# Kernel tuning notes

Hardware: AMD Instinct MI355X
Metric: run time of the kernel (lower is better)

Reference implementation:

```python
import jax, jax.numpy as jnp
import numpy as np

B, N, C, H = 8, 1024, 1024, 16  # batch, seq, dim, heads
HID = 4 * C                     # mlp hidden (mlp_ratio=4.0)


def _ln(x, g, b, eps=1e-5):
    m = x.mean(-1, keepdims=True)
    v = ((x - m) ** 2).mean(-1, keepdims=True)
    return (x - m) / jnp.sqrt(v + eps) * g + b


def setup_inputs() -> dict:
    key = jax.random.key(0)
    ks = jax.random.split(key, 8)
    s = 0.02  # init scale
    f32 = jnp.float32
    return {
        "x": jax.random.normal(ks[0], (B, N, C), f32),
        "g1": jnp.ones((C,), f32), "b1": jnp.zeros((C,), f32),
        "Wq": jax.random.normal(ks[1], (C, C), f32) * s, "bq": jnp.zeros((C,), f32),
        "Wk": jax.random.normal(ks[2], (C, C), f32) * s, "bk": jnp.zeros((C,), f32),
        "Wv": jax.random.normal(ks[3], (C, C), f32) * s, "bv": jnp.zeros((C,), f32),
        "Wp": jax.random.normal(ks[4], (C, C), f32) * s, "bp": jnp.zeros((C,), f32),
        "g2": jnp.ones((C,), f32), "b2": jnp.zeros((C,), f32),
        "W1": jax.random.normal(ks[5], (C, HID), f32) * s, "c1": jnp.zeros((HID,), f32),
        "W2": jax.random.normal(ks[6], (HID, C), f32) * s, "c2": jnp.zeros((C,), f32),
    }


def reference(x, g1, b1, Wq, bq, Wk, bk, Wv, bv, Wp, bp, g2, b2, W1, c1, W2, c2):
    hd = C // H
    scale = hd ** -0.5
    # --- pre-norm self-attention ---
    h = _ln(x, g1, b1)
    # NOTE: faithful to source: direct reshape (B,N,C)->(B,H,N,hd), NOT the
    # standard reshape(B,N,H,hd).transpose -- the original code reshapes the
    # flat N*C block into H contiguous chunks of N*hd.
    q = (h @ Wq + bq).reshape(B, H, -1, hd)
    k = (h @ Wk + bk).reshape(B, H, -1, hd)
    v = (h @ Wv + bv).reshape(B, H, -1, hd)
    attn = jax.nn.softmax(jnp.einsum('bhnd,bhmd->bhnm', q, k) * scale, axis=-1)
    o = jnp.einsum('bhnm,bhmd->bhnd', attn, v)
    o = jnp.swapaxes(o, 1, 2).reshape(B, -1, C)  # (B,N,C)
    x = x + (o @ Wp + bp)
    # --- MLP block ---
    h2 = _ln(x, g2, b2)
    m = jax.nn.gelu(h2 @ W1 + c1, approximate=False) @ W2 + c2
    return x + m
```

## Files before the change

### kernel.cpp

```cpp
#include <hip/hip_runtime.h>
#include <hip/hip_bf16.h>
#include <math.h>

typedef __bf16 bf16_t;
typedef __bf16 bf16x4 __attribute__((ext_vector_type(4)));
typedef __bf16 bf16x8 __attribute__((ext_vector_type(8)));
typedef float  f32x4  __attribute__((ext_vector_type(4)));

typedef __attribute__((address_space(1))) const void GVoid;
typedef __attribute__((address_space(3))) void LVoid;

__device__ __forceinline__ void gld16(const void* g, void* l) {
    __builtin_amdgcn_global_load_lds((GVoid*)g, (LVoid*)l, 16, 0, 0);
}

__device__ __forceinline__ float gelu_exact(float v) {
    return 0.5f * v * (1.0f + erff(v * 0.7071067811865475f));
}

__global__ __launch_bounds__(256) void transpose_f32_bf16(
    const float* __restrict__ in, bf16_t* __restrict__ out,
    int R, int C, size_t inBatch, size_t outBatch)
{
    __shared__ bf16_t tile[64][65];
    const float* src = in  + (size_t)blockIdx.z * inBatch;
    bf16_t*      dst = out + (size_t)blockIdx.z * outBatch;
    const int r0 = blockIdx.y * 64, c0 = blockIdx.x * 64;
    const int t = threadIdx.x, tc = t & 63, tr = t >> 6;
#pragma unroll
    for (int i = 0; i < 16; ++i) {
        int r = tr + i * 4;
        tile[r][tc] = (bf16_t)src[(size_t)(r0 + r) * C + c0 + tc];
    }
    __syncthreads();
#pragma unroll
    for (int i = 0; i < 16; ++i) {
        int r = tr + i * 4;
        dst[(size_t)(c0 + r) * R + r0 + tc] = tile[tc][r];
    }
}

__global__ __launch_bounds__(256) void transpose_bf16(
    const bf16_t* __restrict__ in, bf16_t* __restrict__ out,
    int R, int C, size_t inBatch, size_t outBatch)
{
    __shared__ __align__(16) bf16_t tile[64][65];
    const bf16_t* src = in  + (size_t)blockIdx.z * inBatch;
    bf16_t*       dst = out + (size_t)blockIdx.z * outBatch;
    const int r0 = blockIdx.y * 64, c0 = blockIdx.x * 64;
    const int t = threadIdx.x, tc = t & 63, tr = t >> 6;
#pragma unroll
    for (int i = 0; i < 16; ++i) {
        int r = tr + i * 4;
        tile[r][tc] = src[(size_t)(r0 + r) * C + c0 + tc];
    }
    __syncthreads();
#pragma unroll
    for (int i = 0; i < 16; ++i) {
        int r = tr + i * 4;
        dst[(size_t)(c0 + r) * R + r0 + tc] = tile[tc][r];
    }
}

__global__ __launch_bounds__(256) void ln_kernel(
    const float* __restrict__ x, const float* __restrict__ g,
    const float* __restrict__ b, bf16_t* __restrict__ out)
{
    const int row = blockIdx.x, t = threadIdx.x;
    const float* xr = x + (size_t)row * 1024;
    float v[4];
#pragma unroll
    for (int i = 0; i < 4; ++i) v[i] = xr[t * 4 + i];
    float s = v[0] + v[1] + v[2] + v[3];
    float s2 = v[0]*v[0] + v[1]*v[1] + v[2]*v[2] + v[3]*v[3];
#pragma unroll
    for (int o = 1; o < 64; o <<= 1) { s += __shfl_xor(s, o); s2 += __shfl_xor(s2, o); }
    __shared__ float red[8];
    if ((t & 63) == 0) { red[t >> 6] = s; red[4 + (t >> 6)] = s2; }
    __syncthreads();
    s  = red[0] + red[1] + red[2] + red[3];
    s2 = red[4] + red[5] + red[6] + red[7];
    const float mean = s * (1.f / 1024.f);
    const float var  = fmaxf(s2 * (1.f / 1024.f) - mean * mean, 0.f);
    const float rstd = rsqrtf(var + 1e-5f);
#pragma unroll
    for (int i = 0; i < 4; ++i) {
        int c = t * 4 + i;
        out[(size_t)row * 1024 + c] =
            (bf16_t)((v[i] - mean) * rstd * g[c] + b[c]);
    }
}

template <int MODE>
__global__ __launch_bounds__(256) void gemm_bt(
    const bf16_t* __restrict__ A, const bf16_t* __restrict__ Bt,
    const float* __restrict__ bias, const float* resid_f,
    bf16_t* __restrict__ out_bf, float* out_f, int N, int K)
{
    __shared__ __align__(16) bf16_t As[128 * 32];
    __shared__ __align__(16) bf16_t Bs[128 * 32];
    const int t = threadIdx.x;
    const int wv = t >> 6, ln = t & 63;
    const int wx = wv & 1, wy = wv >> 1;
    const int l16 = ln & 15, quad = ln >> 4;
    const int m0 = blockIdx.x * 128, n0 = blockIdx.y * 128;

    f32x4 acc[4][4];
#pragma unroll
    for (int i = 0; i < 4; ++i)
#pragma unroll
        for (int j = 0; j < 4; ++j) acc[i][j] = f32x4{0.f, 0.f, 0.f, 0.f};

    const int arow = t >> 2;
    const int acol = (t & 3) << 3;
    const bf16_t* gA = A  + (size_t)(m0 + arow) * K + acol;
    const bf16_t* gB = Bt + (size_t)(n0 + arow) * K + acol;
    char* ldsA = (char*)As + wv * 1024;
    char* ldsB = (char*)Bs + wv * 1024;

    for (int kk = 0; kk < K; kk += 32) {
        __syncthreads();
        gld16(gA + kk,                 ldsA);
        gld16(gA + (size_t)64*K + kk,  ldsA + 4096);
        gld16(gB + kk,                 ldsB);
        gld16(gB + (size_t)64*K + kk,  ldsB + 4096);
        __syncthreads();

        bf16x8 af[4], bfr[4];
        const bf16_t* Ab = As + (wy * 64 + l16) * 32 + quad * 8;
        const bf16_t* Bb = Bs + (wx * 64 + l16) * 32 + quad * 8;
#pragma unroll
        for (int i = 0; i < 4; ++i) af[i]  = *(const bf16x8*)(Ab + i * 16 * 32);
#pragma unroll
        for (int j = 0; j < 4; ++j) bfr[j] = *(const bf16x8*)(Bb + j * 16 * 32);
#pragma unroll
        for (int i = 0; i < 4; ++i)
#pragma unroll
            for (int j = 0; j < 4; ++j)
                acc[i][j] = __builtin_amdgcn_mfma_f32_16x16x32_bf16(
                    af[i], bfr[j], acc[i][j], 0, 0, 0);
    }

#pragma unroll
    for (int i = 0; i < 4; ++i) {
        const int rowb = m0 + wy * 64 + i * 16 + quad * 4;
#pragma unroll
        for (int j = 0; j < 4; ++j) {
            const int col = n0 + wx * 64 + j * 16 + l16;
            const float bc = bias[col];
#pragma unroll
            for (int r = 0; r < 4; ++r) {
                const size_t idx = (size_t)(rowb + r) * N + col;
                float vv = acc[i][j][r] + bc;
                if (MODE == 1) out_f[idx] = vv + resid_f[idx];
                else if (MODE == 2) out_bf[idx] = (bf16_t)gelu_exact(vv);
                else out_f[idx] += acc[i][j][r];
            }
        }
    }
}

__global__ __launch_bounds__(256) void gemm_qkv(
    const bf16_t* __restrict__ A, const bf16_t* __restrict__ Bt,
    const float* __restrict__ bq, const float* __restrict__ bk,
    const float* __restrict__ bv,
    bf16_t* __restrict__ Qo, bf16_t* __restrict__ Ko, bf16_t* __restrict__ Vo,
    int K)
{
    __shared__ __align__(16) bf16_t As[128 * 32];
    __shared__ __align__(16) bf16_t Bs[128 * 32];
    const int t = threadIdx.x;
    const int wv = t >> 6, ln = t & 63;
    const int wx = wv & 1, wy = wv >> 1;
    const int l16 = ln & 15, quad = ln >> 4;
    const int m0 = blockIdx.x * 128, n0 = blockIdx.y * 128;

    f32x4 acc[4][4];
#pragma unroll
    for (int i = 0; i < 4; ++i)
#pragma unroll
        for (int j = 0; j < 4; ++j) acc[i][j] = f32x4{0.f, 0.f, 0.f, 0.f};

    const int arow = t >> 2;
    const int acol = (t & 3) << 3;
    const bf16_t* gA = A  + (size_t)(m0 + arow) * K + acol;
    const bf16_t* gB = Bt + (size_t)(n0 + arow) * K + acol;
    char* ldsA = (char*)As + wv * 1024;
    char* ldsB = (char*)Bs + wv * 1024;

    for (int kk = 0; kk < K; kk += 32) {
        __syncthreads();
        gld16(gA + kk,                 ldsA);
        gld16(gA + (size_t)64*K + kk,  ldsA + 4096);
        gld16(gB + kk,                 ldsB);
        gld16(gB + (size_t)64*K + kk,  ldsB + 4096);
        __syncthreads();

        bf16x8 af[4], bfr[4];
        const bf16_t* Ab = As + (wy * 64 + l16) * 32 + quad * 8;
        const bf16_t* Bb = Bs + (wx * 64 + l16) * 32 + quad * 8;
#pragma unroll
        for (int i = 0; i < 4; ++i) af[i]  = *(const bf16x8*)(Ab + i * 16 * 32);
#pragma unroll
        for (int j = 0; j < 4; ++j) bfr[j] = *(const bf16x8*)(Bb + j * 16 * 32);
#pragma unroll
        for (int i = 0; i < 4; ++i)
#pragma unroll
            for (int j = 0; j < 4; ++j)
                acc[i][j] = __builtin_amdgcn_mfma_f32_16x16x32_bf16(
                    af[i], bfr[j], acc[i][j], 0, 0, 0);
    }

    const int which = n0 >> 10;
    const float* bias = which == 0 ? bq : (which == 1 ? bk : bv);
    bf16_t* outp      = which == 0 ? Qo : (which == 1 ? Ko : Vo);
    const int nloc = n0 & 1023;
#pragma unroll
    for (int i = 0; i < 4; ++i) {
        const int rowb = m0 + wy * 64 + i * 16 + quad * 4;
#pragma unroll
        for (int j = 0; j < 4; ++j) {
            const int col = nloc + wx * 64 + j * 16 + l16;
            const float bc = bias[col];
#pragma unroll
            for (int r = 0; r < 4; ++r)
                outp[(size_t)(rowb + r) * 1024 + col] = (bf16_t)(acc[i][j][r] + bc);
        }
    }
}

__global__ __launch_bounds__(256, 2) void attn_kernel(
    const bf16_t* __restrict__ Q, const bf16_t* __restrict__ K,
    const bf16_t* __restrict__ Vt, bf16_t* __restrict__ O)
{
    __shared__ __align__(16) bf16_t smem[26112];
    bf16_t* Vs = smem;
    bf16_t* Ks = smem + 8704;
    bf16_t* Ps = smem + 8704;

    const int t = threadIdx.x;
    const int wv = t >> 6, ln = t & 63;
    const int l16 = ln & 15, quad = ln >> 4;
    const int qt = blockIdx.x, bh = blockIdx.y;
    const size_t hb = (size_t)bh << 16;

    bf16x8 qf[2][2];
#pragma unroll
    for (int rt = 0; rt < 2; ++rt)
#pragma unroll
        for (int ks = 0; ks < 2; ++ks)
            qf[rt][ks] = *(const bf16x8*)(Q + hb +
                (size_t)(qt*128 + wv*32 + rt*16 + l16) * 64 + ks*32 + quad*8);

    float m_run[2] = {-INFINITY, -INFINITY};
    float l_run[2] = {0.f, 0.f};
    f32x4 acc_o[2][4];
#pragma unroll
    for (int rt = 0; rt < 2; ++rt)
#pragma unroll
        for (int dt = 0; dt < 4; ++dt) acc_o[rt][dt] = f32x4{0.f, 0.f, 0.f, 0.f};

    const int krow = t >> 3, kcol = (t & 7) << 3;
    const int vrow = t >> 4, vcol = (t & 15) << 3;
    const float sc = 0.125f;

    for (int j = 0; j < 8; ++j) {
        bf16x8 kg[4], vg[4];
#pragma unroll
        for (int i = 0; i < 4; ++i) {
            kg[i] = *(const bf16x8*)(K  + hb + (size_t)(j*128 + i*32 + krow)*64 + kcol);
            vg[i] = *(const bf16x8*)(Vt + hb + (size_t)(i*16 + vrow)*1024 + j*128 + vcol);
        }
        __syncthreads();
#pragma unroll
        for (int i = 0; i < 4; ++i) {
            *(bf16x8*)(Ks + (i*32 + krow)*72 + kcol)  = kg[i];
            *(bf16x8*)(Vs + (i*16 + vrow)*136 + vcol) = vg[i];
        }
        __syncthreads();

        f32x4 accs[8][2];
#pragma unroll
        for (int nt = 0; nt < 8; ++nt)
#pragma unroll
            for (int rt = 0; rt < 2; ++rt) accs[nt][rt] = f32x4{0.f, 0.f, 0.f, 0.f};
#pragma unroll
        for (int ks = 0; ks < 2; ++ks)
#pragma unroll
            for (int nt = 0; nt < 8; ++nt) {
                bf16x8 kf = *(const bf16x8*)(Ks + (nt*16 + l16)*72 + ks*32 + quad*8);
#pragma unroll
                for (int rt = 0; rt < 2; ++rt)
                    accs[nt][rt] = __builtin_amdgcn_mfma_f32_16x16x32_bf16(
                        kf, qf[rt][ks], accs[nt][rt], 0, 0, 0);
            }

#pragma unroll
        for (int rt = 0; rt < 2; ++rt) {
            float mx = -INFINITY;
#pragma unroll
            for (int nt = 0; nt < 8; ++nt)
#pragma unroll
                for (int r = 0; r < 4; ++r) mx = fmaxf(mx, accs[nt][rt][r]);
            mx *= sc;
            mx = fmaxf(mx, __shfl_xor(mx, 16));
            mx = fmaxf(mx, __shfl_xor(mx, 32));
            const float mnew  = fmaxf(m_run[rt], mx);
            const float alpha = __expf(m_run[rt] - mnew);
            m_run[rt] = mnew;
            float rs = 0.f;
#pragma unroll
            for (int nt = 0; nt < 8; ++nt)
#pragma unroll
                for (int r = 0; r < 4; ++r) {
                    float p = __expf(accs[nt][rt][r] * sc - mnew);
                    accs[nt][rt][r] = p;
                    rs += p;
                }
            rs += __shfl_xor(rs, 16);
            rs += __shfl_xor(rs, 32);
            l_run[rt] = l_run[rt] * alpha + rs;
#pragma unroll
            for (int r = 0; r < 4; ++r) {
                const float af = __shfl(alpha, quad*4 + r, 16);
#pragma unroll
                for (int dt = 0; dt < 4; ++dt) acc_o[rt][dt][r] *= af;
            }
        }

        __syncthreads();
#pragma unroll
        for (int rt = 0; rt < 2; ++rt) {
            const int mrow = wv*32 + rt*16 + l16;
#pragma unroll
            for (int nt = 0; nt < 8; ++nt) {
                bf16x4 pk;
#pragma unroll
                for (int r = 0; r < 4; ++r) pk[r] = (bf16_t)accs[nt][rt][r];
                *(bf16x4*)(Ps + mrow*136 + nt*16 + quad*4) = pk;
            }
        }
#pragma unroll
        for (int ks = 0; ks < 4; ++ks) {
            bf16x8 ap[2];
#pragma unroll
            for (int rt = 0; rt < 2; ++rt)
                ap[rt] = *(const bf16x8*)(Ps + (wv*32 + rt*16 + l16)*136 + ks*32 + quad*8);
#pragma unroll
            for (int dt = 0; dt < 4; ++dt) {
                bf16x8 bvv = *(const bf16x8*)(Vs + (dt*16 + l16)*136 + ks*32 + quad*8);
#pragma unroll
                for (int rt = 0; rt < 2; ++rt)
                    acc_o[rt][dt] = __builtin_amdgcn_mfma_f32_16x16x32_bf16(
                        ap[rt], bvv, acc_o[rt][dt], 0, 0, 0);
            }
        }
    }

    const int b = bh >> 4, h = bh & 15;
#pragma unroll
    for (int rt = 0; rt < 2; ++rt) {
#pragma unroll
        for (int r = 0; r < 4; ++r) {
            const float inv = 1.f / __shfl(l_run[rt], quad*4 + r, 16);
            const int m = qt*128 + wv*32 + rt*16 + quad*4 + r;
#pragma unroll
            for (int dt = 0; dt < 4; ++dt) {
                const int d = dt*16 + l16;
                O[((size_t)b*1024 + m)*1024 + h*64 + d] =
                    (bf16_t)(acc_o[rt][dt][r] * inv);
            }
        }
    }
}

extern "C" void kernel_launch(void* const* d_in, const int* in_sizes, int n_in,
                              void* d_out, int out_size, void* d_ws, size_t ws_size,
                              hipStream_t stream)
{
    (void)in_sizes; (void)n_in;
    const size_t MB = 1ull << 20;
    if (ws_size < 64 * MB) {
        hipMemsetAsync(d_out, 0, (size_t)out_size * sizeof(float), stream);
        return;
    }

    const float* x  = (const float*)d_in[0];
    const float* g1 = (const float*)d_in[1];
    const float* b1 = (const float*)d_in[2];
    const float* Wq = (const float*)d_in[3];
    const float* bq = (const float*)d_in[4];
    const float* Wk = (const float*)d_in[5];
    const float* bk = (const float*)d_in[6];
    const float* Wv = (const float*)d_in[7];
    const float* bv = (const float*)d_in[8];
    const float* Wp = (const float*)d_in[9];
    const float* bp = (const float*)d_in[10];
    const float* g2 = (const float*)d_in[11];
    const float* b2 = (const float*)d_in[12];
    const float* W1 = (const float*)d_in[13];
    const float* c1 = (const float*)d_in[14];
    const float* W2 = (const float*)d_in[15];
    const float* c2 = (const float*)d_in[16];

    char* ws = (char*)d_ws;
    bf16_t* Kb  = (bf16_t*)(ws);
    bf16_t* Vb  = (bf16_t*)(ws + 16 * MB);
    bf16_t* Cs  = (bf16_t*)(ws + 32 * MB);
    bf16_t* WqT = (bf16_t*)(ws + 48 * MB);
    bf16_t* WpT = (bf16_t*)(ws + 54 * MB);
    bf16_t* W1T = (bf16_t*)(ws + 56 * MB);
    bf16_t* W2T = (bf16_t*)(ws + 48 * MB);
    bf16_t* Qb  = (bf16_t*)d_out;
    bf16_t* Ob  = Vb;
    bf16_t* hid = Kb;
    bf16_t* h2  = Cs;
    float*  x2  = (float*)d_out;
    float*  outf = (float*)d_out;

    const dim3 blk(256);

    transpose_f32_bf16<<<dim3(16, 16, 1), blk, 0, stream>>>(Wq, WqT,              1024, 1024, 0, 0);
    transpose_f32_bf16<<<dim3(16, 16, 1), blk, 0, stream>>>(Wk, WqT + 1024*1024,  1024, 1024, 0, 0);
    transpose_f32_bf16<<<dim3(16, 16, 1), blk, 0, stream>>>(Wv, WqT + 2*1024*1024, 1024, 1024, 0, 0);
    transpose_f32_bf16<<<dim3(16, 16, 1), blk, 0, stream>>>(Wp, WpT,              1024, 1024, 0, 0);
    transpose_f32_bf16<<<dim3(64, 16, 1), blk, 0, stream>>>(W1, W1T,              1024, 4096, 0, 0);

    ln_kernel<<<8192, blk, 0, stream>>>(x, g1, b1, Cs);

    gemm_qkv<<<dim3(64, 24), blk, 0, stream>>>(Cs, WqT, bq, bk, bv, Qb, Kb, Vb, 1024);

    transpose_bf16<<<dim3(1, 16, 128), blk, 0, stream>>>(Vb, Cs, 1024, 64, 65536, 65536);

    attn_kernel<<<dim3(8, 128), blk, 0, stream>>>(Qb, Kb, Cs, Ob);

    gemm_bt<1><<<dim3(64, 8), blk, 0, stream>>>(Ob, WpT, bp, x, nullptr, x2, 1024, 1024);

    transpose_f32_bf16<<<dim3(16, 32, 2), blk, 0, stream>>>(
        W2, W2T, 2048, 1024, 2048*1024, 2048*1024);

    ln_kernel<<<8192, blk, 0, stream>>>(x2, g2, b2, h2);

    for (int c = 0; c < 2; ++c) {
        gemm_bt<2><<<dim3(64, 16), blk, 0, stream>>>(
            h2, W1T + (size_t)c * 2048 * 1024, c1 + c * 2048, nullptr,
            hid, nullptr, 2048, 1024);
        if (c == 0)
            gemm_bt<1><<<dim3(64, 8), blk, 0, stream>>>(
                hid, W2T, c2, outf, nullptr, outf, 1024, 2048);
        else
            gemm_bt<5><<<dim3(64, 8), blk, 0, stream>>>(
                hid, W2T + (size_t)2048 * 1024, c2, nullptr, nullptr,
                outf, 1024, 2048);
    }
}
```

Measured before the change: 615.9 us.

## Replace GEMMs with 256x256 double-buffered swizzled-LDS MFMA kernel; vectorize layernorm

All projection and MLP GEMMs now use one templated kernel with 512 threads, 256x256 output tiles and 64-wide K steps. It double-buffers LDS with async global-to-LDS loads, XOR-swizzles LDS rows to avoid bank conflicts, and splits MFMA work into four phases with barriers, s_setprio and a prefetch of tile k+2. The larger tiles raise arithmetic intensity and the pipelining hides load latency. In exchange it uses 128KB of LDS, a large accumulator register footprint and fewer blocks (e.g. 128 for the N=1024 GEMMs), which may underfill the GPU. Layernorm loads and stores are also vectorized to float4/bf16x4.

```diff
diff --git a/kernel.cpp b/kernel.cpp
--- a/kernel.cpp
+++ b/kernel.cpp
@@ -67,10 +67,8 @@
     const float* __restrict__ b, bf16_t* __restrict__ out)
 {
     const int row = blockIdx.x, t = threadIdx.x;
-    const float* xr = x + (size_t)row * 1024;
-    float v[4];
-#pragma unroll
-    for (int i = 0; i < 4; ++i) v[i] = xr[t * 4 + i];
+    const float4 v4 = ((const float4*)(x + (size_t)row * 1024))[t];
+    float v[4] = {v4.x, v4.y, v4.z, v4.w};
     float s = v[0] + v[1] + v[2] + v[3];
     float s2 = v[0]*v[0] + v[1]*v[1] + v[2]*v[2] + v[3]*v[3];
 #pragma unroll
@@ -83,148 +81,188 @@
     const float mean = s * (1.f / 1024.f);
     const float var  = fmaxf(s2 * (1.f / 1024.f) - mean * mean, 0.f);
     const float rstd = rsqrtf(var + 1e-5f);
-#pragma unroll
-    for (int i = 0; i < 4; ++i) {
-        int c = t * 4 + i;
-        out[(size_t)row * 1024 + c] =
-            (bf16_t)((v[i] - mean) * rstd * g[c] + b[c]);
-    }
+    const float4 g4 = ((const float4*)g)[t];
+    const float4 b4 = ((const float4*)b)[t];
+    bf16x4 o;
+    o[0] = (bf16_t)((v[0] - mean) * rstd * g4.x + b4.x);
+    o[1] = (bf16_t)((v[1] - mean) * rstd * g4.y + b4.y);
+    o[2] = (bf16_t)((v[2] - mean) * rstd * g4.z + b4.z);
+    o[3] = (bf16_t)((v[3] - mean) * rstd * g4.w + b4.w);
+    *(bf16x4*)(out + (size_t)row * 1024 + t * 4) = o;
+}
+
+__device__ __forceinline__ bf16x8 lds_rd(const char* base, int rl, int colB) {
+    return *(const bf16x8*)(base + rl * 128 + (colB ^ ((rl & 7) << 4)));
 }
 
 template <int MODE>
-__global__ __launch_bounds__(256) void gemm_bt(
+__global__ __launch_bounds__(512, 2) void gemm256(
     const bf16_t* __restrict__ A, const bf16_t* __restrict__ Bt,
-    const float* __restrict__ bias, const float* resid_f,
-    bf16_t* __restrict__ out_bf, float* out_f, int N, int K)
-{
-    __shared__ __align__(16) bf16_t As[128 * 32];
-    __shared__ __align__(16) bf16_t Bs[128 * 32];
+    const float* __restrict__ b0, const float* __restrict__ b1,
+    const float* __restrict__ b2, const float* resid,
+    bf16_t* __restrict__ ob0, bf16_t* __restrict__ ob1,
+    bf16_t* __restrict__ ob2, float* of,
+    int N, int K)
+{
+    __shared__ __align__(16) char lds[131072];
     const int t = threadIdx.x;
-    const int wv = t >> 6, ln = t & 63;
-    const int wx = wv & 1, wy = wv >> 1;
+    const int w = t >> 6, ln = t & 63;
+    const int wm = w >> 2, wn = w & 3;
     const int l16 = ln & 15, quad = ln >> 4;
-    const int m0 = blockIdx.x * 128, n0 = blockIdx.y * 128;
-
-    f32x4 acc[4][4];
-#pragma unroll
-    for (int i = 0; i < 4; ++i)
+    const int m0 = blockIdx.x * 256, n0 = blockIdx.y * 256;
+
+    const bf16_t* gA = A  + (size_t)m0 * K;
+    const bf16_t* gB = Bt + (size_t)n0 * K;
+
+    const int w1k  = w << 10;
+    const int srow = t >> 3;
+    const int scol = ((t & 7) ^ (srow & 7)) << 3;
+
+    auto stage = [&](int kt, int dbuf) {
+        char* aL = (char*)lds + dbuf * 32768 + w1k;
+        char* bL = (char*)lds + 65536 + dbuf * 32768 + w1k;
+#pragma unroll
+        for (int h = 0; h < 2; ++h) {
+#pragma unroll
+            for (int r2 = 0; r2 < 2; ++r2) {
+                const int row = h * 128 + r2 * 64 + srow;
+                gld16(gA + (size_t)row * K + kt + scol, aL + h * 16384 + r2 * 8192);
+                gld16(gB + (size_t)row * K + kt + scol, bL + h * 16384 + r2 * 8192);
+            }
+        }
+    };
+
+    f32x4 acc[8][4];
+#pragma unroll
+    for (int i = 0; i < 8; ++i)
 #pragma unroll
         for (int j = 0; j < 4; ++j) acc[i][j] = f32x4{0.f, 0.f, 0.f, 0.f};
 
-    const int arow = t >> 2;
-    const int acol = (t & 3) << 3;
-    const bf16_t* gA = A  + (size_t)(m0 + arow) * K + acol;
-    const bf16_t* gB = Bt + (size_t)(n0 + arow) * K + acol;
-    char* ldsA = (char*)As + wv * 1024;
-    char* ldsB = (char*)Bs + wv * 1024;
-
-    for (int kk = 0; kk < K; kk += 32) {
-        __syncthreads();
-        gld16(gA + kk,                 ldsA);
-        gld16(gA + (size_t)64*K + kk,  ldsA + 4096);
-        gld16(gB + kk,                 ldsB);
-        gld16(gB + (size_t)64*K + kk,  ldsB + 4096);
-        __syncthreads();
-
-        bf16x8 af[4], bfr[4];
-        const bf16_t* Ab = As + (wy * 64 + l16) * 32 + quad * 8;
-        const bf16_t* Bb = Bs + (wx * 64 + l16) * 32 + quad * 8;
-#pragma unroll
-        for (int i = 0; i < 4; ++i) af[i]  = *(const bf16x8*)(Ab + i * 16 * 32);
-#pragma unroll
-        for (int j = 0; j < 4; ++j) bfr[j] = *(const bf16x8*)(Bb + j * 16 * 32);
-#pragma unroll
-        for (int i = 0; i < 4; ++i)
-#pragma unroll
-            for (int j = 0; j < 4; ++j)
-                acc[i][j] = __builtin_amdgcn_mfma_f32_16x16x32_bf16(
-                    af[i], bfr[j], acc[i][j], 0, 0, 0);
-    }
-
-#pragma unroll
-    for (int i = 0; i < 4; ++i) {
-        const int rowb = m0 + wy * 64 + i * 16 + quad * 4;
+    const int ktiles = K >> 6;
+    stage(0, 0);
+    stage(64, 1);
+    asm volatile("s_waitcnt vmcnt(8)" ::: "memory");
+    __builtin_amdgcn_s_barrier();
+    __builtin_amdgcn_sched_barrier(0);
+
+    bf16x8 af[4][2], bfr[4][2];
+
+    for (int kt = 0; kt < ktiles; ++kt) {
+        const int b = kt & 1;
+        const char* aB = (const char*)lds + b * 32768 + wm * 16384;
+        const char* bB = (const char*)lds + 65536 + b * 32768 + (wn >> 1) * 16384;
+        const int bR0 = (wn & 1) << 6;
+
+#pragma unroll
+        for (int i = 0; i < 4; ++i)
+#pragma unroll
+            for (int ks = 0; ks < 2; ++ks)
+                af[i][ks] = lds_rd(aB, i * 16 + l16, ks * 64 + quad * 16);
+#pragma unroll
+        for (int j = 0; j < 2; ++j)
+#pragma unroll
+            for (int ks = 0; ks < 2; ++ks)
+                bfr[j][ks] = lds_rd(bB, bR0 + j * 16 + l16, ks * 64 + quad * 16);
+        __builtin_amdgcn_s_setprio(1);
+#pragma unroll
+        for (int i = 0; i < 4; ++i)
+#pragma unroll
+            for (int j = 0; j < 2; ++j)
+#pragma unroll
+                for (int ks = 0; ks < 2; ++ks)
+                    acc[i][j] = __builtin_amdgcn_mfma_f32_16x16x32_bf16(
+                        af[i][ks], bfr[j][ks], acc[i][j], 0, 0, 0);
+        __builtin_amdgcn_s_setprio(0);
+        __builtin_amdgcn_sched_barrier(0);
+        __builtin_amdgcn_s_barrier();
+
+#pragma unroll
+        for (int j = 2; j < 4; ++j)
+#pragma unroll
+            for (int ks = 0; ks < 2; ++ks)
+                bfr[j][ks] = lds_rd(bB, bR0 + j * 16 + l16, ks * 64 + quad * 16);
+        __builtin_amdgcn_s_setprio(1);
+#pragma unroll
+        for (int i = 0; i < 4; ++i)
+#pragma unroll
+            for (int j = 2; j < 4; ++j)
+#pragma unroll
+                for (int ks = 0; ks < 2; ++ks)
+                    acc[i][j] = __builtin_amdgcn_mfma_f32_16x16x32_bf16(
+                        af[i][ks], bfr[j][ks], acc[i][j], 0, 0, 0);
+        __builtin_amdgcn_s_setprio(0);
+        __builtin_amdgcn_sched_barrier(0);
+        __builtin_amdgcn_s_barrier();
+
+#pragma unroll
+        for (int i = 0; i < 4; ++i)
+#pragma unroll
+            for (int ks = 0; ks < 2; ++ks)
+                af[i][ks] = lds_rd(aB, 64 + i * 16 + l16, ks * 64 + quad * 16);
+        __builtin_amdgcn_s_setprio(1);
+#pragma unroll
+        for (int i = 0; i < 4; ++i)
+#pragma unroll
+            for (int j = 2; j < 4; ++j)
+#pragma unroll
+                for (int ks = 0; ks < 2; ++ks)
+                    acc[4 + i][j] = __builtin_amdgcn_mfma_f32_16x16x32_bf16(
+                        af[i][ks], bfr[j][ks], acc[4 + i][j], 0, 0, 0);
+        __builtin_amdgcn_s_setprio(0);
+        __builtin_amdgcn_sched_barrier(0);
+        asm volatile("s_waitcnt vmcnt(0)" ::: "memory");
+        __builtin_amdgcn_s_barrier();
+        __builtin_amdgcn_sched_barrier(0);
+
+        if (kt + 2 < ktiles) stage((kt + 2) << 6, b);
+        __builtin_amdgcn_s_setprio(1);
+#pragma unroll
+        for (int i = 0; i < 4; ++i)
+#pragma unroll
+            for (int j = 0; j < 2; ++j)
+#pragma unroll
+                for (int ks = 0; ks < 2; ++ks)
+                    acc[4 + i][j] = __builtin_amdgcn_mfma_f32_16x16x32_bf16(
+                        af[i][ks], bfr[j][ks], acc[4 + i][j], 0, 0, 0);
+        __builtin_amdgcn_s_setprio(0);
+        __builtin_amdgcn_sched_barrier(0);
+    }
+
+#pragma unroll
+    for (int i = 0; i < 8; ++i) {
+        const int rowb = m0 + wm * 128 + i * 16 + quad * 4;
 #pragma unroll
         for (int j = 0; j < 4; ++j) {
-            const int col = n0 + wx * 64 + j * 16 + l16;
-            const float bc = bias[col];
-#pragma unroll
-            for (int r = 0; r < 4; ++r) {
-                const size_t idx = (size_t)(rowb + r) * N + col;
-                float vv = acc[i][j][r] + bc;
-                if (MODE == 1) out_f[idx] = vv + resid_f[idx];
-                else if (MODE == 2) out_bf[idx] = (bf16_t)gelu_exact(vv);
-                else out_f[idx] += acc[i][j][r];
-            }
-        }
-    }
-}
-
-__global__ __launch_bounds__(256) void gemm_qkv(
-    const bf16_t* __restrict__ A, const bf16_t* __restrict__ Bt,
-    const float* __restrict__ bq, const float* __restrict__ bk,
-    const float* __restrict__ bv,
-    bf16_t* __restrict__ Qo, bf16_t* __restrict__ Ko, bf16_t* __restrict__ Vo,
-    int K)
-{
-    __shared__ __align__(16) bf16_t As[128 * 32];
-    __shared__ __align__(16) bf16_t Bs[128 * 32];
-    const int t = threadIdx.x;
-    const int wv = t >> 6, ln = t & 63;
-    const int wx = wv & 1, wy = wv >> 1;
-    const int l16 = ln & 15, quad = ln >> 4;
-    const int m0 = blockIdx.x * 128, n0 = blockIdx.y * 128;
-
-    f32x4 acc[4][4];
-#pragma unroll
-    for (int i = 0; i < 4; ++i)
-#pragma unroll
-        for (int j = 0; j < 4; ++j) acc[i][j] = f32x4{0.f, 0.f, 0.f, 0.f};
-
-    const int arow = t >> 2;
-    const int acol = (t & 3) << 3;
-    const bf16_t* gA = A  + (size_t)(m0 + arow) * K + acol;
-    const bf16_t* gB = Bt + (size_t)(n0 + arow) * K + acol;
-    char* ldsA = (char*)As + wv * 1024;
-    char* ldsB = (char*)Bs + wv * 1024;
-
-    for (int kk = 0; kk < K; kk += 32) {
-        __syncthreads();
-        gld16(gA + kk,                 ldsA);
-        gld16(gA + (size_t)64*K + kk,  ldsA + 4096);
-        gld16(gB + kk,                 ldsB);
-        gld16(gB + (size_t)64*K + kk,  ldsB + 4096);
-        __syncthreads();
-
-        bf16x8 af[4], bfr[4];
-        const bf16_t* Ab = As + (wy * 64 + l16) * 32 + quad * 8;
-        const bf16_t* Bb = Bs + (wx * 64 + l16) * 32 + quad * 8;
-#pragma unroll
-        for (int i = 0; i < 4; ++i) af[i]  = *(const bf16x8*)(Ab + i * 16 * 32);
-#pragma unroll
-        for (int j = 0; j < 4; ++j) bfr[j] = *(const bf16x8*)(Bb + j * 16 * 32);
-#pragma unroll
-        for (int i = 0; i < 4; ++i)
-#pragma unroll
-            for (int j = 0; j < 4; ++j)
-                acc[i][j] = __builtin_amdgcn_mfma_f32_16x16x32_bf16(
-                    af[i], bfr[j], acc[i][j], 0, 0, 0);
-    }
-
-    const int which = n0 >> 10;
-    const float* bias = which == 0 ? bq : (which == 1 ? bk : bv);
-    bf16_t* outp      = which == 0 ? Qo : (which == 1 ? Ko : Vo);
-    const int nloc = n0 & 1023;
-#pragma unroll
-    for (int i = 0; i < 4; ++i) {
-        const int rowb = m0 + wy * 64 + i * 16 + quad * 4;
-#pragma unroll
-        for (int j = 0; j < 4; ++j) {
-            const int col = nloc + wx * 64 + j * 16 + l16;
-            const float bc = bias[col];
-#pragma unroll
-            for (int r = 0; r < 4; ++r)
-                outp[(size_t)(rowb + r) * 1024 + col] = (bf16_t)(acc[i][j][r] + bc);
+            const int col = n0 + wn * 64 + j * 16 + l16;
+            if (MODE == 0) {
+                const int which = col >> 10;
+                const float* bias = which == 0 ? b0 : (which == 1 ? b1 : b2);
+                bf16_t* outp      = which == 0 ? ob0 : (which == 1 ? ob1 : ob2);
+                const int cl = col & 1023;
+                const float bc = bias[cl];
+#pragma unroll
+                for (int r = 0; r < 4; ++r)
+                    outp[(size_t)(rowb + r) * 1024 + cl] = (bf16_t)(acc[i][j][r] + bc);
+            } else if (MODE == 1) {
+                const float bc = b0[col];
+#pragma unroll
+                for (int r = 0; r < 4; ++r) {
+                    const size_t idx = (size_t)(rowb + r) * N + col;
+                    of[idx] = acc[i][j][r] + bc + resid[idx];
+                }
+            } else if (MODE == 2) {
+                const float bc = b0[col];
+#pragma unroll
+                for (int r = 0; r < 4; ++r)
+                    ob0[(size_t)(rowb + r) * N + col] =
+                        (bf16_t)gelu_exact(acc[i][j][r] + bc);
+            } else {
+#pragma unroll
+                for (int r = 0; r < 4; ++r) {
+                    const size_t idx = (size_t)(rowb + r) * N + col;
+                    of[idx] += acc[i][j][r];
+                }
+            }
         }
     }
 }
@@ -419,6 +457,7 @@
     float*  outf = (float*)d_out;
 
     const dim3 blk(256);
+    const dim3 blk5(512);
 
     transpose_f32_bf16<<<dim3(16, 16, 1), blk, 0, stream>>>(Wq, WqT,              1024, 1024, 0, 0);
     transpose_f32_bf16<<<dim3(16, 16, 1), blk, 0, stream>>>(Wk, WqT + 1024*1024,  1024, 1024, 0, 0);
@@ -428,13 +467,15 @@
 
     ln_kernel<<<8192, blk, 0, stream>>>(x, g1, b1, Cs);
 
-    gemm_qkv<<<dim3(64, 24), blk, 0, stream>>>(Cs, WqT, bq, bk, bv, Qb, Kb, Vb, 1024);
+    gemm256<0><<<dim3(32, 12), blk5, 0, stream>>>(
+        Cs, WqT, bq, bk, bv, nullptr, Qb, Kb, Vb, nullptr, 3072, 1024);
 
     transpose_bf16<<<dim3(1, 16, 128), blk, 0, stream>>>(Vb, Cs, 1024, 64, 65536, 65536);
 
     attn_kernel<<<dim3(8, 128), blk, 0, stream>>>(Qb, Kb, Cs, Ob);
 
-    gemm_bt<1><<<dim3(64, 8), blk, 0, stream>>>(Ob, WpT, bp, x, nullptr, x2, 1024, 1024);
+    gemm256<1><<<dim3(32, 4), blk5, 0, stream>>>(
+        Ob, WpT, bp, nullptr, nullptr, x, nullptr, nullptr, nullptr, x2, 1024, 1024);
 
     transpose_f32_bf16<<<dim3(16, 32, 2), blk, 0, stream>>>(
         W2, W2T, 2048, 1024, 2048*1024, 2048*1024);
@@ -442,15 +483,16 @@
     ln_kernel<<<8192, blk, 0, stream>>>(x2, g2, b2, h2);
 
     for (int c = 0; c < 2; ++c) {
-        gemm_bt<2><<<dim3(64, 16), blk, 0, stream>>>(
-            h2, W1T + (size_t)c * 2048 * 1024, c1 + c * 2048, nullptr,
-            hid, nullptr, 2048, 1024);
+        gemm256<2><<<dim3(32, 8), blk5, 0, stream>>>(
+            h2, W1T + (size_t)c * 2048 * 1024, c1 + c * 2048,
+            nullptr, nullptr, nullptr, hid, nullptr, nullptr, nullptr, 2048, 1024);
         if (c == 0)
-            gemm_bt<1><<<dim3(64, 8), blk, 0, stream>>>(
-                hid, W2T, c2, outf, nullptr, outf, 1024, 2048);
+            gemm256<1><<<dim3(32, 4), blk5, 0, stream>>>(
+                hid, W2T, c2, nullptr, nullptr, outf,
+                nullptr, nullptr, nullptr, outf, 1024, 2048);
         else
-            gemm_bt<5><<<dim3(64, 8), blk, 0, stream>>>(
-                hid, W2T + (size_t)2048 * 1024, c2, nullptr, nullptr,
-                outf, 1024, 2048);
-    }
-}
+            gemm256<5><<<dim3(32, 4), blk5, 0, stream>>>(
+                hid, W2T + (size_t)2048 * 1024, nullptr, nullptr, nullptr, nullptr,
+                nullptr, nullptr, nullptr, outf, 1024, 2048);
+    }
+}
```

New measurement: 611.0 us. Within noise of the previous version (-0.8%).
